# Optimization experiments

Measured on AMD Instinct MI355X. Metric: run time of the kernel, lower is better.

The kernel has to match this reference:

```python
import jax, jax.numpy as jnp
import numpy as np

B, S, HID, NH, DH, L, FF = 1, 4096, 768, 12, 64, 12, 3072
WIN = 256       # one-sided sliding window (attention_window = 512 total)
NG = 16         # number of global-attention tokens
VOCAB = 50265
NEG = -1e9


def layer_norm(x, g, b, eps=1e-5):
    mu = jnp.mean(x, -1, keepdims=True)
    var = jnp.mean((x - mu) ** 2, -1, keepdims=True)
    return (x - mu) * jax.lax.rsqrt(var + eps) * g + b


def forward(input_ids, attention_mask, global_attention_mask, tok_emb, pos_emb,
            emb_ln_w, emb_ln_b, Wqkv, bqkv, Wo, bo, ln1_w, ln1_b,
            W1, b1, W2, b2, ln2_w, ln2_b, cls_W, cls_b):
    c = WIN
    nc = S // c
    amask = attention_mask.astype(jnp.float32)          # [B,S]
    gmask = global_attention_mask.astype(jnp.float32)   # [B,S]

    # --- static-shape helpers for the sparse pattern ---
    # key chunk k covers padded positions [k*c, k*c + 3c)
    idx = (jnp.arange(nc) * c)[:, None] + jnp.arange(3 * c)[None, :]      # [nc,3c]
    diff = jnp.arange(3 * c)[None, :] - c - jnp.arange(c)[:, None]        # [c,3c]
    band = jnp.abs(diff) <= c
    mp = jnp.pad(amask, ((0, 0), (c, c)))[:, idx]                         # [B,nc,3c]
    gp = jnp.pad(gmask, ((0, 0), (c, c)))[:, idx]
    key_ok = (mp > 0) & (gp == 0)           # local keys: valid and not global (globals handled separately)
    loc_valid = band[None, None] & key_ok[:, :, None, :]                  # [B,nc,c,3c]

    # indices of the NG global tokens (earliest first)
    _, gidx = jax.lax.top_k(gmask * (2.0 * S) - jnp.arange(S, dtype=jnp.float32), NG)
    gvalid = jnp.take_along_axis(gmask, gidx, axis=1)                     # [B,NG]

    def attn(x, Wqkv_l, bqkv_l, Wo_l, bo_l):
        qkv = x @ Wqkv_l + bqkv_l
        q, k, v = jnp.split(qkv, 3, axis=-1)
        hd = lambda t: t.reshape(B, S, NH, DH).transpose(0, 2, 1, 3)      # [B,nh,S,dh]
        q = hd(q) * (DH ** -0.5); k = hd(k); v = hd(v)

        # sliding-window (banded) attention via overlapping key chunks
        kp = jnp.pad(k, ((0, 0), (0, 0), (c, c), (0, 0)))
        vp = jnp.pad(v, ((0, 0), (0, 0), (c, c), (0, 0)))
        Kc, Vc = kp[:, :, idx], vp[:, :, idx]                             # [B,nh,nc,3c,dh]
        Qc = q.reshape(B, NH, nc, c, DH)
        s_loc = jnp.einsum('bhkpd,bhkqd->bhkpq', Qc, Kc)                  # [B,nh,nc,c,3c]
        s_loc = jnp.where(loc_valid[:, None], s_loc, NEG)

        # every token also attends to the global tokens
        gi = jnp.broadcast_to(gidx[:, None, :, None], (B, NH, NG, DH))
        Kg = jnp.take_along_axis(k, gi, axis=2)                           # [B,nh,NG,dh]
        Vg = jnp.take_along_axis(v, gi, axis=2)
        Qg = jnp.take_along_axis(q, gi, axis=2)
        s_glb = jnp.einsum('bhkpd,bhgd->bhkpg', Qc, Kg)                   # [B,nh,nc,c,NG]
        s_glb = jnp.where(gvalid[:, None, None, None, :] > 0, s_glb, NEG)

        p = jax.nn.softmax(jnp.concatenate([s_loc, s_glb], -1), axis=-1)
        o = (jnp.einsum('bhkpq,bhkqd->bhkpd', p[..., :3 * c], Vc)
             + jnp.einsum('bhkpg,bhgd->bhkpd', p[..., 3 * c:], Vg))
        o = o.reshape(B, NH, S, DH).transpose(0, 2, 1, 3)                 # [B,S,nh,dh]

        # global tokens attend to the full sequence
        s_full = jnp.einsum('bhgd,bhsd->bhgs', Qg, k)
        s_full = jnp.where(amask[:, None, None, :] > 0, s_full, NEG)
        og = jnp.einsum('bhgs,bhsd->bhgd', jax.nn.softmax(s_full, -1), v)
        og = og.transpose(0, 2, 1, 3)                                     # [B,NG,nh,dh]
        bi = jnp.arange(B)[:, None]
        o = o.at[bi, gidx].set(jnp.where(gvalid[..., None, None] > 0, og, o[bi, gidx]))
        return o.reshape(B, S, HID) @ Wo_l + bo_l

    h = layer_norm(tok_emb[input_ids] + pos_emb[None], emb_ln_w, emb_ln_b)

    def step(h, p):
        Wq, bq, Wo_l, bo_l, g1, bl1, w1, bb1, w2, bb2, g2, bl2 = p
        h = layer_norm(h + attn(h, Wq, bq, Wo_l, bo_l), g1, bl1)          # post-LN, RoBERTa-style
        f = jax.nn.gelu(h @ w1 + bb1, approximate=False) @ w2 + bb2
        h = layer_norm(h + f, g2, bl2)
        return h, None

    h, _ = jax.lax.scan(step, h, (Wqkv, bqkv, Wo, bo, ln1_w, ln1_b,
                                  W1, b1, W2, b2, ln2_w, ln2_b))
    m = amask[..., None]
    pooled = (h * m).sum(1) / m.sum(1)           # masked mean-pool; dropout is eval no-op
    return pooled @ cls_W + cls_b                # [B,2] logits


def setup_inputs():
    key = jax.random.key(0)
    ks = jax.random.split(key, 8)
    nrm = lambda k, shp: jax.random.normal(k, shp, jnp.float32) * 0.02
    return dict(
        input_ids=jax.random.randint(ks[0], (B, S), 0, VOCAB),
        attention_mask=jnp.ones((B, S), jnp.int32),
        global_attention_mask=jnp.concatenate(
            [jnp.ones((B, NG), jnp.int32), jnp.zeros((B, S - NG), jnp.int32)], axis=1),
        tok_emb=nrm(ks[1], (VOCAB, HID)),
        pos_emb=nrm(ks[2], (S, HID)),
        emb_ln_w=jnp.ones((HID,)), emb_ln_b=jnp.zeros((HID,)),
        Wqkv=nrm(ks[3], (L, HID, 3 * HID)), bqkv=jnp.zeros((L, 3 * HID)),
        Wo=nrm(ks[4], (L, HID, HID)), bo=jnp.zeros((L, HID)),
        ln1_w=jnp.ones((L, HID)), ln1_b=jnp.zeros((L, HID)),
        W1=nrm(ks[5], (L, HID, FF)), b1=jnp.zeros((L, FF)),
        W2=nrm(ks[6], (L, FF, HID)), b2=jnp.zeros((L, HID)),
        ln2_w=jnp.ones((L, HID)), ln2_b=jnp.zeros((L, HID)),
        cls_W=nrm(ks[7], (HID, 2)), cls_b=jnp.zeros((2,)),
    )


def reference(input_ids, attention_mask, global_attention_mask, tok_emb, pos_emb,
              emb_ln_w, emb_ln_b, Wqkv, bqkv, Wo, bo, ln1_w, ln1_b,
              W1, b1, W2, b2, ln2_w, ln2_b, cls_W, cls_b):
    return forward(input_ids, attention_mask, global_attention_mask, tok_emb, pos_emb,
                   emb_ln_w, emb_ln_b, Wqkv, bqkv, Wo, bo, ln1_w, ln1_b,
                   W1, b1, W2, b2, ln2_w, ln2_b, cls_W, cls_b)
```

## Files before the change

kernel.cpp:

```cpp
#include <hip/hip_runtime.h>
#include <cmath>

#define S 4096
#define HID 768
#define NH 12
#define DH 64
#define CHUNK 256
#define NC (S / CHUNK)
#define NG 16
#define FF 3072
#define NLAYER 12
#define QKV3 (3 * HID)
#define NEGV -1e9f

typedef _Float16 f16;
typedef __attribute__((ext_vector_type(2))) _Float16 f16x2;
typedef __attribute__((ext_vector_type(4))) _Float16 f16x4;
typedef __attribute__((ext_vector_type(8))) _Float16 f16x8;
typedef __attribute__((ext_vector_type(4))) float f32x4;

__device__ __forceinline__ void async16(f16* lds, const f16* g) {
  __builtin_amdgcn_global_load_lds((const __attribute__((address_space(1))) unsigned int*)g,
                                   (__attribute__((address_space(3))) unsigned int*)lds,
                                   16, 0, 0);
}

__device__ __forceinline__ int xcd_swz(int lin, int nwg) {
  return (lin & 7) * (nwg >> 3) + (lin >> 3);
}

__device__ __forceinline__ float block_reduce_sum(float v, float* red) {
  int t = threadIdx.x;
  red[t] = v; __syncthreads();
  for (int st = 128; st > 0; st >>= 1) {
    if (t < st) red[t] += red[t + st];
    __syncthreads();
  }
  float r = red[0]; __syncthreads();
  return r;
}

__global__ void gidx_kernel(const int* __restrict__ gmask, int* __restrict__ gidx,
                            float* __restrict__ gvalid) {
  if (threadIdx.x != 0 || blockIdx.x != 0) return;
  int cnt = 0;
  for (int s = 0; s < S && cnt < NG; s++)
    if (gmask[s] > 0) { gidx[cnt] = s; gvalid[cnt] = 1.f; cnt++; }
  for (int s = 0; s < S && cnt < NG; s++)
    if (gmask[s] == 0) { gidx[cnt] = s; gvalid[cnt] = 0.f; cnt++; }
}

__global__ __launch_bounds__(256) void embed_ln_kernel(
    const int* __restrict__ ids, const float* __restrict__ tok,
    const float* __restrict__ pos, const float* __restrict__ g,
    const float* __restrict__ b, f16* __restrict__ h16) {
  int s = blockIdx.x, t = threadIdx.x;
  __shared__ float xs[HID];
  __shared__ float red[256];
  const float* tr = tok + (size_t)ids[s] * HID;
  const float* pr = pos + (size_t)s * HID;
  float ls = 0.f;
  for (int i = t; i < HID; i += 256) { float v = tr[i] + pr[i]; xs[i] = v; ls += v; }
  float mu = block_reduce_sum(ls, red) * (1.f / HID);
  float lv = 0.f;
  for (int i = t; i < HID; i += 256) { float d = xs[i] - mu; lv += d * d; }
  float var = block_reduce_sum(lv, red) * (1.f / HID);
  float inv = rsqrtf(var + 1e-5f);
  for (int i = t; i < HID; i += 256)
    h16[(size_t)s * HID + i] = (f16)((xs[i] - mu) * inv * g[i] + b[i]);
}

__global__ __launch_bounds__(256) void ln_kernel(
    const f16* __restrict__ sum16, const float* __restrict__ g,
    const float* __restrict__ b, f16* __restrict__ h16) {
  int s = blockIdx.x, t = threadIdx.x;
  __shared__ float red[256];
  float x0 = (float)sum16[(size_t)s * HID + t];
  float x1 = (float)sum16[(size_t)s * HID + t + 256];
  float x2 = (float)sum16[(size_t)s * HID + t + 512];
  float mu = block_reduce_sum(x0 + x1 + x2, red) * (1.f / HID);
  float d0 = x0 - mu, d1 = x1 - mu, d2 = x2 - mu;
  float var = block_reduce_sum(d0 * d0 + d1 * d1 + d2 * d2, red) * (1.f / HID);
  float inv = rsqrtf(var + 1e-5f);
  h16[(size_t)s * HID + t] = (f16)(d0 * inv * g[t] + b[t]);
  h16[(size_t)s * HID + t + 256] = (f16)(d1 * inv * g[t + 256] + b[t + 256]);
  h16[(size_t)s * HID + t + 512] = (f16)(d2 * inv * g[t + 512] + b[t + 512]);
}

__global__ __launch_bounds__(256) void wt_kernel(const float* __restrict__ W,
                                                 f16* __restrict__ WT, int K, int N) {
  size_t lo = (size_t)blockIdx.z * K * N;
  const float* Wl = W + lo;
  f16* WTl = WT + lo;
  __shared__ float tile[32][33];
  int k0 = blockIdx.y * 32, n0 = blockIdx.x * 32;
  int t = threadIdx.x;
  int r = t >> 3, c = (t & 7) * 4;
  float4 v = *(const float4*)&Wl[(size_t)(k0 + r) * N + n0 + c];
  tile[r][c] = v.x; tile[r][c + 1] = v.y; tile[r][c + 2] = v.z; tile[r][c + 3] = v.w;
  __syncthreads();
  int n = t >> 3, kq = (t & 7) * 4;
  f16x4 o = {(f16)tile[kq][n], (f16)tile[kq + 1][n], (f16)tile[kq + 2][n], (f16)tile[kq + 3][n]};
  *(f16x4*)&WTl[(size_t)(n0 + n) * K + k0 + kq] = o;
}

#define GBK 64

template <bool GELU>
__global__ __launch_bounds__(256) void gemm_f16_kernel(
    const f16* __restrict__ A, const f16* __restrict__ BT,
    const float* __restrict__ bias, f16* __restrict__ Cout, int M, int N, int K) {
  __shared__ f16 As[128 * GBK];
  __shared__ f16 Bs[128 * GBK];
  int t = threadIdx.x, lane = t & 63, wave = t >> 6;
  int wr = wave >> 1, wc = wave & 1;
  int gx = gridDim.x;
  int nl = xcd_swz(blockIdx.y * gx + blockIdx.x, gx * gridDim.y);
  int bx = nl % gx, by = nl / gx;

  f32x4 acc[4][4];
#pragma unroll
  for (int mi = 0; mi < 4; mi++)
#pragma unroll
    for (int ni = 0; ni < 4; ni++) acc[mi][ni] = (f32x4){0.f, 0.f, 0.f, 0.f};

  const f16* Ablk = A + (size_t)(by * 128) * K;
  const f16* Bblk = BT + (size_t)(bx * 128) * K;
  int rl = lane >> 3;
  int lc = (lane & 7) ^ rl;

  for (int k0 = 0; k0 < K; k0 += GBK) {
#pragma unroll
    for (int ii = 0; ii < 4; ii++) {
      int i = wave * 4 + ii;
      int r = i * 8 + rl;
      async16(&As[i * 512], Ablk + (size_t)r * K + k0 + lc * 8);
      async16(&Bs[i * 512], Bblk + (size_t)r * K + k0 + lc * 8);
    }
    __syncthreads();
#pragma unroll
    for (int kc = 0; kc < 2; kc++) {
      f16x8 af[4], bf[4];
#pragma unroll
      for (int mi = 0; mi < 4; mi++) {
        int row = wr * 64 + mi * 16 + (lane & 15);
        int pc = (kc * 4 + (lane >> 4)) ^ (row & 7);
        af[mi] = *(const f16x8*)&As[row * 64 + pc * 8];
      }
#pragma unroll
      for (int ni = 0; ni < 4; ni++) {
        int row = wc * 64 + ni * 16 + (lane & 15);
        int pc = (kc * 4 + (lane >> 4)) ^ (row & 7);
        bf[ni] = *(const f16x8*)&Bs[row * 64 + pc * 8];
      }
#pragma unroll
      for (int mi = 0; mi < 4; mi++)
#pragma unroll
        for (int ni = 0; ni < 4; ni++)
          acc[mi][ni] = __builtin_amdgcn_mfma_f32_16x16x32_f16(af[mi], bf[ni], acc[mi][ni], 0, 0, 0);
    }
    __syncthreads();
  }

  int row_base = by * 128 + wr * 64 + (lane >> 4) * 4;
  int col_base = bx * 128 + wc * 64 + (lane & 15);
#pragma unroll
  for (int mi = 0; mi < 4; mi++) {
#pragma unroll
    for (int ni = 0; ni < 4; ni++) {
      int col = col_base + ni * 16;
      float bs = bias[col];
#pragma unroll
      for (int j = 0; j < 4; j++) {
        int row = row_base + mi * 16 + j;
        float x = acc[mi][ni][j] + bs;
        if (GELU) x = 0.5f * x * (1.f + erff(x * 0.70710678118654752f));
        Cout[(size_t)row * N + col] = (f16)x;
      }
    }
  }
}

template <bool RESID>
__global__ __launch_bounds__(256) void gemm_f16_n64_kernel(
    const f16* __restrict__ A, const f16* __restrict__ BT,
    const float* __restrict__ bias, const f16* __restrict__ resid,
    f16* __restrict__ Cout, int M, int N, int K) {
  __shared__ f16 As[128 * GBK];
  __shared__ f16 Bs[64 * GBK];
  int t = threadIdx.x, lane = t & 63, wave = t >> 6;
  int wr = wave >> 1, wc = wave & 1;
  int gx = gridDim.x;
  int nl = xcd_swz(blockIdx.y * gx + blockIdx.x, gx * gridDim.y);
  int bx = nl % gx, by = nl / gx;

  f32x4 acc[4][2];
#pragma unroll
  for (int mi = 0; mi < 4; mi++)
#pragma unroll
    for (int ni = 0; ni < 2; ni++) acc[mi][ni] = (f32x4){0.f, 0.f, 0.f, 0.f};

  const f16* Ablk = A + (size_t)(by * 128) * K;
  const f16* Bblk = BT + (size_t)(bx * 64) * K;
  int rl = lane >> 3;
  int lc = (lane & 7) ^ rl;

  for (int k0 = 0; k0 < K; k0 += GBK) {
#pragma unroll
    for (int ii = 0; ii < 4; ii++) {
      int i = wave * 4 + ii;
      int r = i * 8 + rl;
      async16(&As[i * 512], Ablk + (size_t)r * K + k0 + lc * 8);
    }
#pragma unroll
    for (int ii = 0; ii < 2; ii++) {
      int i = wave * 2 + ii;
      int r = i * 8 + rl;
      async16(&Bs[i * 512], Bblk + (size_t)r * K + k0 + lc * 8);
    }
    __syncthreads();
#pragma unroll
    for (int kc = 0; kc < 2; kc++) {
      f16x8 af[4], bf[2];
#pragma unroll
      for (int mi = 0; mi < 4; mi++) {
        int row = wr * 64 + mi * 16 + (lane & 15);
        int pc = (kc * 4 + (lane >> 4)) ^ (row & 7);
        af[mi] = *(const f16x8*)&As[row * 64 + pc * 8];
      }
#pragma unroll
      for (int ni = 0; ni < 2; ni++) {
        int row = wc * 32 + ni * 16 + (lane & 15);
        int pc = (kc * 4 + (lane >> 4)) ^ (row & 7);
        bf[ni] = *(const f16x8*)&Bs[row * 64 + pc * 8];
      }
#pragma unroll
      for (int mi = 0; mi < 4; mi++)
#pragma unroll
        for (int ni = 0; ni < 2; ni++)
          acc[mi][ni] = __builtin_amdgcn_mfma_f32_16x16x32_f16(af[mi], bf[ni], acc[mi][ni], 0, 0, 0);
    }
    __syncthreads();
  }

  int row_base = by * 128 + wr * 64 + (lane >> 4) * 4;
  int col_base = bx * 64 + wc * 32 + (lane & 15);
#pragma unroll
  for (int mi = 0; mi < 4; mi++) {
#pragma unroll
    for (int ni = 0; ni < 2; ni++) {
      int col = col_base + ni * 16;
      float bs = bias[col];
#pragma unroll
      for (int j = 0; j < 4; j++) {
        int row = row_base + mi * 16 + j;
        float x = acc[mi][ni][j] + bs;
        if (RESID) x += (float)resid[(size_t)row * N + col];
        Cout[(size_t)row * N + col] = (f16)x;
      }
    }
  }
}

#define ROWP 72

__global__ __launch_bounds__(256) void local_attn_mfma_kernel(
    const f16* __restrict__ qkv, const int* __restrict__ amask,
    const int* __restrict__ gmask, const int* __restrict__ gidx,
    const float* __restrict__ gvalid, f16* __restrict__ outp) {
  int nl = xcd_swz(blockIdx.x, NH * 64);
  int h = nl >> 6;
  int qb = nl & 63;
  int q0 = qb * 64;
  int t = threadIdx.x, lane = t & 63, w = t >> 6;
  int g4 = lane >> 4, l15 = lane & 15;

  __shared__ f16 Qs[64 * ROWP];
  __shared__ f16 Kt[64 * ROWP];
  __shared__ f16 Vt[64 * ROWP];
  __shared__ f16 Pb[4 * 16 * ROWP];
  __shared__ unsigned kokLo, kokHi;
  __shared__ float gvs[NG];

  {
    int r = t >> 2, c2 = (t & 3) * 2;
    const f16* qr = qkv + (size_t)(q0 + r) * QKV3 + h * DH + c2 * 8;
    f16x8 v0 = *(const f16x8*)qr;
    f16x8 v1 = *(const f16x8*)(qr + 8);
#pragma unroll
    for (int e = 0; e < 8; e++) { v0[e] = v0[e] * (f16)0.125f; v1[e] = v1[e] * (f16)0.125f; }
    *(f16x8*)&Qs[r * ROWP + c2 * 8] = v0;
    *(f16x8*)&Qs[r * ROWP + c2 * 8 + 8] = v1;
    if (t < NG) gvs[t] = gvalid[t];
  }
  __syncthreads();

  int qrow = w * 16 + l15;
  f16x8 qf0 = *(const f16x8*)&Qs[qrow * ROWP + g4 * 8];
  f16x8 qf1 = *(const f16x8*)&Qs[qrow * ROWP + 32 + g4 * 8];

  float mb = -50000.f, lp = 0.f;
  f32x4 oacc[4];
#pragma unroll
  for (int sd = 0; sd < 4; sd++) oacc[sd] = (f32x4){0.f, 0.f, 0.f, 0.f};

  f16* Pw = &Pb[w * 16 * ROWP];

  for (int kt = 0; kt <= 9; kt++) {
    int jb = q0 - 256 + kt * 64;
    bool isG = (kt == 9);
    if (!isG && (jb + 64 <= 0 || jb >= S)) continue;
    __syncthreads();
    {
      int k = t >> 2, c2 = (t & 3) * 2;
      int j = isG ? (k < NG ? gidx[k] : -1) : (jb + k);
      bool jv = isG ? (k < NG && gvs[k] > 0.f) : (j >= 0 && j < S);
      f16x8 v0 = {}, v1 = {};
      if (jv) {
        const f16* kr = qkv + (size_t)j * QKV3 + HID + h * DH + c2 * 8;
        v0 = *(const f16x8*)kr; v1 = *(const f16x8*)(kr + 8);
      }
      *(f16x8*)&Kt[k * ROWP + c2 * 8] = v0;
      *(f16x8*)&Kt[k * ROWP + c2 * 8 + 8] = v1;
    }
    if (w == 0) {
      int k = lane;
      bool ok;
      if (isG) ok = (k < NG && gvs[k] > 0.f);
      else {
        int j = jb + k;
        ok = (j >= 0 && j < S) && (amask[j] != 0) && (gmask[j] == 0);
      }
      unsigned long long m = __ballot(ok);
      if (lane == 0) { kokLo = (unsigned)m; kokHi = (unsigned)(m >> 32); }
    }
    {
      int k2 = (t & 31) * 2, dq = (t >> 5) * 8;
      int j0 = isG ? (k2 < NG ? gidx[k2] : -1) : (jb + k2);
      int j1 = isG ? (k2 + 1 < NG ? gidx[k2 + 1] : -1) : (jb + k2 + 1);
      bool ok0 = isG ? (k2 < NG && gvs[k2] > 0.f) : (j0 >= 0 && j0 < S);
      bool ok1 = isG ? (k2 + 1 < NG && gvs[k2 + 1] > 0.f) : (j1 >= 0 && j1 < S);
      f16x8 va = {}, vb = {};
      if (ok0) va = *(const f16x8*)(qkv + (size_t)j0 * QKV3 + 2 * HID + h * DH + dq);
      if (ok1) vb = *(const f16x8*)(qkv + (size_t)j1 * QKV3 + 2 * HID + h * DH + dq);
#pragma unroll
      for (int e = 0; e < 8; e++) {
        f16x2 pr = {va[e], vb[e]};
        *(f16x2*)&Vt[(dq + e) * ROWP + k2] = pr;
      }
    }
    __syncthreads();

    unsigned long long kok = ((unsigned long long)kokHi << 32) | (unsigned long long)kokLo;

    f32x4 sv[4];
    __builtin_amdgcn_s_setprio(1);
#pragma unroll
    for (int s4 = 0; s4 < 4; s4++) {
      int krow = s4 * 16 + l15;
      f16x8 ka0 = *(const f16x8*)&Kt[krow * ROWP + g4 * 8];
      f16x8 ka1 = *(const f16x8*)&Kt[krow * ROWP + 32 + g4 * 8];
      f32x4 a = {0.f, 0.f, 0.f, 0.f};
      a = __builtin_amdgcn_mfma_f32_16x16x32_f16(ka0, qf0, a, 0, 0, 0);
      a = __builtin_amdgcn_mfma_f32_16x16x32_f16(ka1, qf1, a, 0, 0, 0);
      sv[s4] = a;
    }
    __builtin_amdgcn_s_setprio(0);
    int ql = w * 16 + l15;
#pragma unroll
    for (int s4 = 0; s4 < 4; s4++)
#pragma unroll
      for (int r = 0; r < 4; r++) {
        int kl = s4 * 16 + g4 * 4 + r;
        bool ok = (kok >> kl) & 1ull;
        if (kt == 0) ok = ok && (kl >= ql);
        else if (kt == 8) ok = ok && (kl <= ql);
        sv[s4][r] = ok ? sv[s4][r] : -1e30f;
      }
    float mt = -1e30f;
#pragma unroll
    for (int s4 = 0; s4 < 4; s4++)
#pragma unroll
      for (int r = 0; r < 4; r++) mt = fmaxf(mt, sv[s4][r]);
    mt = fmaxf(mt, __shfl_xor(mt, 16));
    mt = fmaxf(mt, __shfl_xor(mt, 32));
    float mn = fmaxf(mb, mt);
    float corr = __expf(mb - mn);
    mb = mn;
    lp *= corr;
#pragma unroll
    for (int sd = 0; sd < 4; sd++)
#pragma unroll
      for (int r = 0; r < 4; r++) oacc[sd][r] *= corr;
#pragma unroll
    for (int s4 = 0; s4 < 4; s4++) {
#pragma unroll
      for (int rp = 0; rp < 2; rp++) {
        float p0 = __expf(sv[s4][rp * 2] - mn);
        float p1 = __expf(sv[s4][rp * 2 + 1] - mn);
        f16 h0 = (f16)p0, h1 = (f16)p1;
        lp += (float)h0 + (float)h1;
        int kl = s4 * 16 + g4 * 4 + rp * 2;
        f16x2 pr = {h0, h1};
        *(f16x2*)&Pw[l15 * ROWP + kl] = pr;
      }
    }
    f16x8 pf0 = *(const f16x8*)&Pw[l15 * ROWP + g4 * 8];
    f16x8 pf1 = *(const f16x8*)&Pw[l15 * ROWP + 32 + g4 * 8];
    __builtin_amdgcn_s_setprio(1);
#pragma unroll
    for (int sd = 0; sd < 4; sd++) {
      int drow = sd * 16 + l15;
      f16x8 va0 = *(const f16x8*)&Vt[drow * ROWP + g4 * 8];
      f16x8 va1 = *(const f16x8*)&Vt[drow * ROWP + 32 + g4 * 8];
      oacc[sd] = __builtin_amdgcn_mfma_f32_16x16x32_f16(va0, pf0, oacc[sd], 0, 0, 0);
      oacc[sd] = __builtin_amdgcn_mfma_f32_16x16x32_f16(va1, pf1, oacc[sd], 0, 0, 0);
    }
    __builtin_amdgcn_s_setprio(0);
  }

  float lt = lp + __shfl_xor(lp, 16);
  lt = lt + __shfl_xor(lt, 32);
  float inv = (lt > 0.f) ? 1.f / lt : 0.f;
  int qg = q0 + w * 16 + l15;
  f16* orow = outp + (size_t)qg * HID + h * DH;
#pragma unroll
  for (int sd = 0; sd < 4; sd++)
#pragma unroll
    for (int r = 0; r < 4; r++)
      orow[sd * 16 + g4 * 4 + r] = (f16)(oacc[sd][r] * inv);
}

__global__ __launch_bounds__(256) void gscore_kernel(
    const f16* __restrict__ qkv, const int* __restrict__ amask,
    const int* __restrict__ gidx, float* __restrict__ Sg, float2* __restrict__ cstat) {
  int h = blockIdx.x >> 4, jc = blockIdx.x & 15;
  int t = threadIdx.x, lane = t & 63, w = t >> 6;
  __shared__ f16 Qs[NG][DH];
  __shared__ float wred[4][NG];
  __shared__ float cmaxs[NG];
  if (t < 128) {
    int g = t >> 3, c = (t & 7) * 8;
    const f16* qr = qkv + (size_t)gidx[g] * QKV3 + h * DH + c;
    *(f16x8*)&Qs[g][c] = *(const f16x8*)qr;
  }
  __syncthreads();
  int j = jc * 256 + t;
  const f16x8* kr = (const f16x8*)(qkv + (size_t)j * QKV3 + HID + h * DH);
  f16x8 kv[8];
#pragma unroll
  for (int c = 0; c < 8; c++) kv[c] = kr[c];
  bool ok = amask[j] != 0;
  float sg[NG];
#pragma unroll 4
  for (int g = 0; g < NG; g++) {
    float s = 0.f;
#pragma unroll
    for (int c = 0; c < 8; c++) {
      f16x8 qv = *(const f16x8*)&Qs[g][c * 8];
#pragma unroll
      for (int e = 0; e < 8; e++) s += (float)qv[e] * (float)kv[c][e];
    }
    sg[g] = ok ? s * 0.125f : NEGV;
    Sg[(size_t)(h * NG + g) * S + j] = sg[g];
  }
#pragma unroll
  for (int g = 0; g < NG; g++) {
    float m = sg[g];
#pragma unroll
    for (int st = 1; st < 64; st <<= 1) m = fmaxf(m, __shfl_xor(m, st));
    if (lane == 0) wred[w][g] = m;
  }
  __syncthreads();
  if (t < NG)
    cmaxs[t] = fmaxf(fmaxf(wred[0][t], wred[1][t]), fmaxf(wred[2][t], wred[3][t]));
  __syncthreads();
#pragma unroll
  for (int g = 0; g < NG; g++) {
    float p = __expf(sg[g] - cmaxs[g]);
#pragma unroll
    for (int st = 1; st < 64; st <<= 1) p += __shfl_xor(p, st);
    if (lane == 0) wred[w][g] = p;
  }
  __syncthreads();
  if (t < NG) {
    float s4 = wred[0][t] + wred[1][t] + wred[2][t] + wred[3][t];
    cstat[((size_t)(h * NG + t)) * 16 + jc] = make_float2(cmaxs[t], s4);
  }
}

__global__ __launch_bounds__(256) void gpv_kernel(
    const f16* __restrict__ qkv, const float* __restrict__ Sg,
    const float2* __restrict__ cstat, float* __restrict__ part) {
  int h = blockIdx.x >> 4, jc = blockIdx.x & 15;
  int jb = jc * 256;
  int t = threadIdx.x;
  __shared__ float Ps[NG][256];
  __shared__ f16 Vs[256][DH];
  __shared__ float ms[NG], dinv[NG];
  if (t < NG) {
    const float2* cs = &cstat[((size_t)(h * NG + t)) * 16];
    float m = -1e30f;
#pragma unroll
    for (int c = 0; c < 16; c++) m = fmaxf(m, cs[c].x);
    float den = 0.f;
#pragma unroll
    for (int c = 0; c < 16; c++) den += cs[c].y * __expf(cs[c].x - m);
    ms[t] = m;
    dinv[t] = den > 0.f ? 1.f / den : 0.f;
  }
  __syncthreads();
#pragma unroll
  for (int g = 0; g < NG; g++)
    Ps[g][t] = __expf(Sg[(size_t)(h * NG + g) * S + jb + t] - ms[g]) * dinv[g];
  {
    int r = t >> 3, c = (t & 7) * 8;
#pragma unroll
    for (int pp = 0; pp < 8; pp++) {
      int row = pp * 32 + r;
      const f16* vr = qkv + (size_t)(jb + row) * QKV3 + 2 * HID + h * DH + c;
      *(f16x8*)&Vs[row][c] = *(const f16x8*)vr;
    }
  }
  __syncthreads();
  int d = t & 63, g4 = t >> 6;
  float o0 = 0.f, o1 = 0.f, o2 = 0.f, o3 = 0.f;
#pragma unroll 8
  for (int j = 0; j < 256; j++) {
    float v = (float)Vs[j][d];
    o0 += Ps[g4][j] * v;
    o1 += Ps[g4 + 4][j] * v;
    o2 += Ps[g4 + 8][j] * v;
    o3 += Ps[g4 + 12][j] * v;
  }
  size_t base = ((size_t)h * NG) * 16 * 64;
  part[base + ((size_t)(g4) * 16 + jc) * 64 + d] = o0;
  part[base + ((size_t)(g4 + 4) * 16 + jc) * 64 + d] = o1;
  part[base + ((size_t)(g4 + 8) * 16 + jc) * 64 + d] = o2;
  part[base + ((size_t)(g4 + 12) * 16 + jc) * 64 + d] = o3;
}

__global__ __launch_bounds__(64) void gout_kernel(
    const float* __restrict__ part, const int* __restrict__ gidx,
    const float* __restrict__ gvalid, f16* __restrict__ attn16) {
  int h = blockIdx.x >> 4, g = blockIdx.x & 15;
  if (gvalid[g] <= 0.f) return;
  int d = threadIdx.x;
  const float* pr = part + (((size_t)(h * NG + g)) * 16) * 64 + d;
  float s = 0.f;
#pragma unroll
  for (int jc = 0; jc < 16; jc++) s += pr[jc * 64];
  attn16[(size_t)gidx[g] * HID + h * DH + d] = (f16)s;
}

__global__ __launch_bounds__(256) void pool_part_kernel(
    const f16* __restrict__ h, const int* __restrict__ amask, float* __restrict__ part) {
  int b = blockIdx.x, t = threadIdx.x;
  float a0 = 0.f, a1 = 0.f, a2 = 0.f;
  for (int r = 0; r < 64; r++) {
    int s = b * 64 + r;
    float w = (float)amask[s];
    const f16* hr = h + (size_t)s * HID;
    a0 += (float)hr[t] * w;
    a1 += (float)hr[t + 256] * w;
    a2 += (float)hr[t + 512] * w;
  }
  part[(size_t)b * HID + t] = a0;
  part[(size_t)b * HID + t + 256] = a1;
  part[(size_t)b * HID + t + 512] = a2;
}

__global__ __launch_bounds__(256) void cls_head_kernel(
    const float* __restrict__ part, const int* __restrict__ amask,
    const float* __restrict__ clsW, const float* __restrict__ clsb,
    float* __restrict__ out) {
  __shared__ float pooled[HID];
  __shared__ float red[256];
  int t = threadIdx.x;
  for (int i = t; i < HID; i += 256) {
    float s = 0.f;
    for (int b2 = 0; b2 < 64; b2++) s += part[(size_t)b2 * HID + i];
    pooled[i] = s;
  }
  float c = 0.f;
  for (int s2 = t; s2 < S; s2 += 256) c += (float)amask[s2];
  float cnt = block_reduce_sum(c, red);
  float p0 = 0.f, p1 = 0.f;
  for (int i = t; i < HID; i += 256) {
    float pv = pooled[i] / cnt;
    p0 += pv * clsW[i * 2];
    p1 += pv * clsW[i * 2 + 1];
  }
  float s0 = block_reduce_sum(p0, red);
  float s1 = block_reduce_sum(p1, red);
  if (t == 0) { out[0] = s0 + clsb[0]; out[1] = s1 + clsb[1]; }
}

extern "C" void kernel_launch(void* const* d_in, const int* in_sizes, int n_in,
                              void* d_out, int out_size, void* d_ws, size_t ws_size,
                              hipStream_t stream) {
  const int* ids = (const int*)d_in[0];
  const int* amask = (const int*)d_in[1];
  const int* gmask = (const int*)d_in[2];
  const float* tok = (const float*)d_in[3];
  const float* pos = (const float*)d_in[4];
  const float* elnw = (const float*)d_in[5];
  const float* elnb = (const float*)d_in[6];
  const float* Wqkv = (const float*)d_in[7];
  const float* bqkv = (const float*)d_in[8];
  const float* Wo = (const float*)d_in[9];
  const float* bo = (const float*)d_in[10];
  const float* ln1w = (const float*)d_in[11];
  const float* ln1b = (const float*)d_in[12];
  const float* W1 = (const float*)d_in[13];
  const float* b1 = (const float*)d_in[14];
  const float* W2 = (const float*)d_in[15];
  const float* b2 = (const float*)d_in[16];
  const float* ln2w = (const float*)d_in[17];
  const float* ln2b = (const float*)d_in[18];
  const float* clsW = (const float*)d_in[19];
  const float* clsb = (const float*)d_in[20];

  char* w8 = (char*)d_ws;
  size_t o = 0;
  f16* h16 = (f16*)(w8 + o); o += (size_t)S * HID * 2;
  f16* qkv16 = (f16*)(w8 + o); o += (size_t)S * QKV3 * 2;
  f16* attn16 = (f16*)(w8 + o); o += (size_t)S * HID * 2;
  f16* ff16 = (f16*)(w8 + o); o += (size_t)S * FF * 2;
  f16* sum16 = (f16*)(w8 + o); o += (size_t)S * HID * 2;
  float* part = (float*)(w8 + o); o += (size_t)64 * HID * 4;
  int* gidx = (int*)(w8 + o); o += 64;
  float* gvalid = (float*)(w8 + o); o += 64;
  f16* WqkvT = (f16*)(w8 + o); o += (size_t)NLAYER * HID * QKV3 * 2;
  f16* WoT = (f16*)(w8 + o); o += (size_t)NLAYER * HID * HID * 2;
  f16* W1T = (f16*)(w8 + o); o += (size_t)NLAYER * HID * FF * 2;
  f16* W2T = (f16*)(w8 + o); o += (size_t)NLAYER * FF * HID * 2;
  float* Sg = (float*)(w8 + o); o += (size_t)NH * NG * S * 4;
  float2* cstat = (float2*)(w8 + o); o += (size_t)NH * NG * 16 * 8;
  float* gpart = (float*)(w8 + o); o += (size_t)NH * NG * 16 * 64 * 4;

  gidx_kernel<<<1, 64, 0, stream>>>(gmask, gidx, gvalid);
  embed_ln_kernel<<<S, 256, 0, stream>>>(ids, tok, pos, elnw, elnb, h16);
  wt_kernel<<<dim3(QKV3 / 32, HID / 32, NLAYER), 256, 0, stream>>>(Wqkv, WqkvT, HID, QKV3);
  wt_kernel<<<dim3(HID / 32, HID / 32, NLAYER), 256, 0, stream>>>(Wo, WoT, HID, HID);
  wt_kernel<<<dim3(FF / 32, HID / 32, NLAYER), 256, 0, stream>>>(W1, W1T, HID, FF);
  wt_kernel<<<dim3(HID / 32, FF / 32, NLAYER), 256, 0, stream>>>(W2, W2T, FF, HID);

  for (int l = 0; l < NLAYER; l++) {
    gemm_f16_kernel<false><<<dim3(QKV3 / 128, S / 128), 256, 0, stream>>>(
        h16, WqkvT + (size_t)l * HID * QKV3, bqkv + (size_t)l * QKV3, qkv16, S, QKV3, HID);
    local_attn_mfma_kernel<<<NH * 64, 256, 0, stream>>>(
        qkv16, amask, gmask, gidx, gvalid, attn16);
    gscore_kernel<<<NH * 16, 256, 0, stream>>>(qkv16, amask, gidx, Sg, cstat);
    gpv_kernel<<<NH * 16, 256, 0, stream>>>(qkv16, Sg, cstat, gpart);
    gout_kernel<<<NH * NG, 64, 0, stream>>>(gpart, gidx, gvalid, attn16);
    gemm_f16_n64_kernel<true><<<dim3(HID / 64, S / 128), 256, 0, stream>>>(
        attn16, WoT + (size_t)l * HID * HID, bo + (size_t)l * HID, h16, sum16, S, HID, HID);
    ln_kernel<<<S, 256, 0, stream>>>(sum16, ln1w + (size_t)l * HID, ln1b + (size_t)l * HID, h16);
    gemm_f16_kernel<true><<<dim3(FF / 128, S / 128), 256, 0, stream>>>(
        h16, W1T + (size_t)l * HID * FF, b1 + (size_t)l * FF, ff16, S, FF, HID);
    gemm_f16_n64_kernel<true><<<dim3(HID / 64, S / 128), 256, 0, stream>>>(
        ff16, W2T + (size_t)l * FF * HID, b2 + (size_t)l * HID, h16, sum16, S, HID, FF);
    ln_kernel<<<S, 256, 0, stream>>>(sum16, ln2w + (size_t)l * HID, ln2b + (size_t)l * HID, h16);
  }
  pool_part_kernel<<<64, 256, 0, stream>>>(h16, amask, part);
  cls_head_kernel<<<1, 256, 0, stream>>>(part, amask, clsW, clsb, (float*)d_out);
}
```

Measured before the change: 2.547 ms.

## Split-K the FFN2 GEMM with fused reduce+LN, and prefetch attention K/V tiles

Result: faster. 2.332 ms (-8.5%).

```diff
diff --git a/kernel.cpp b/kernel.cpp
--- a/kernel.cpp
+++ b/kernel.cpp
@@ -87,6 +87,27 @@
   h16[(size_t)s * HID + t + 512] = (f16)(d2 * inv * g[t + 512] + b[t + 512]);
 }
 
+__global__ __launch_bounds__(256) void ln_ffn2_kernel(
+    const f16* __restrict__ p0, const f16* __restrict__ p1,
+    const float* __restrict__ bias, const float* __restrict__ g,
+    const float* __restrict__ b, f16* __restrict__ h16) {
+  int s = blockIdx.x, t = threadIdx.x;
+  __shared__ float red[256];
+  size_t base = (size_t)s * HID;
+  float x0 = (float)p0[base + t] + (float)p1[base + t] + bias[t] + (float)h16[base + t];
+  float x1 = (float)p0[base + t + 256] + (float)p1[base + t + 256] + bias[t + 256] +
+             (float)h16[base + t + 256];
+  float x2 = (float)p0[base + t + 512] + (float)p1[base + t + 512] + bias[t + 512] +
+             (float)h16[base + t + 512];
+  float mu = block_reduce_sum(x0 + x1 + x2, red) * (1.f / HID);
+  float d0 = x0 - mu, d1 = x1 - mu, d2 = x2 - mu;
+  float var = block_reduce_sum(d0 * d0 + d1 * d1 + d2 * d2, red) * (1.f / HID);
+  float inv = rsqrtf(var + 1e-5f);
+  h16[base + t] = (f16)(d0 * inv * g[t] + b[t]);
+  h16[base + t + 256] = (f16)(d1 * inv * g[t + 256] + b[t + 256]);
+  h16[base + t + 512] = (f16)(d2 * inv * g[t + 512] + b[t + 512]);
+}
+
 __global__ __launch_bounds__(256) void wt_kernel(const float* __restrict__ W,
                                                  f16* __restrict__ WT, int K, int N) {
   size_t lo = (size_t)blockIdx.z * K * N;
@@ -262,7 +283,114 @@
   }
 }
 
+__global__ __launch_bounds__(256) void gemm_f16_n64_splitk_kernel(
+    const f16* __restrict__ A, const f16* __restrict__ BT,
+    f16* __restrict__ p0, f16* __restrict__ p1, int M, int N, int K) {
+  __shared__ f16 As[128 * GBK];
+  __shared__ f16 Bs[64 * GBK];
+  int t = threadIdx.x, lane = t & 63, wave = t >> 6;
+  int wr = wave >> 1, wc = wave & 1;
+  int gx = gridDim.x;
+  int nl = xcd_swz(blockIdx.y * gx + blockIdx.x, gx * gridDim.y);
+  int bx = nl % gx, by = nl / gx;
+  int kz = blockIdx.z;
+  int KH = K >> 1;
+  f16* pout = kz ? p1 : p0;
+
+  f32x4 acc[4][2];
+#pragma unroll
+  for (int mi = 0; mi < 4; mi++)
+#pragma unroll
+    for (int ni = 0; ni < 2; ni++) acc[mi][ni] = (f32x4){0.f, 0.f, 0.f, 0.f};
+
+  const f16* Ablk = A + (size_t)(by * 128) * K + (size_t)kz * KH;
+  const f16* Bblk = BT + (size_t)(bx * 64) * K + (size_t)kz * KH;
+  int rl = lane >> 3;
+  int lc = (lane & 7) ^ rl;
+
+  for (int k0 = 0; k0 < KH; k0 += GBK) {
+#pragma unroll
+    for (int ii = 0; ii < 4; ii++) {
+      int i = wave * 4 + ii;
+      int r = i * 8 + rl;
+      async16(&As[i * 512], Ablk + (size_t)r * K + k0 + lc * 8);
+    }
+#pragma unroll
+    for (int ii = 0; ii < 2; ii++) {
+      int i = wave * 2 + ii;
+      int r = i * 8 + rl;
+      async16(&Bs[i * 512], Bblk + (size_t)r * K + k0 + lc * 8);
+    }
+    __syncthreads();
+#pragma unroll
+    for (int kc = 0; kc < 2; kc++) {
+      f16x8 af[4], bf[2];
+#pragma unroll
+      for (int mi = 0; mi < 4; mi++) {
+        int row = wr * 64 + mi * 16 + (lane & 15);
+        int pc = (kc * 4 + (lane >> 4)) ^ (row & 7);
+        af[mi] = *(const f16x8*)&As[row * 64 + pc * 8];
+      }
+#pragma unroll
+      for (int ni = 0; ni < 2; ni++) {
+        int row = wc * 32 + ni * 16 + (lane & 15);
+        int pc = (kc * 4 + (lane >> 4)) ^ (row & 7);
+        bf[ni] = *(const f16x8*)&Bs[row * 64 + pc * 8];
+      }
+#pragma unroll
+      for (int mi = 0; mi < 4; mi++)
+#pragma unroll
+        for (int ni = 0; ni < 2; ni++)
+          acc[mi][ni] = __builtin_amdgcn_mfma_f32_16x16x32_f16(af[mi], bf[ni], acc[mi][ni], 0, 0, 0);
+    }
+    __syncthreads();
+  }
+
+  int row_base = by * 128 + wr * 64 + (lane >> 4) * 4;
+  int col_base = bx * 64 + wc * 32 + (lane & 15);
+#pragma unroll
+  for (int mi = 0; mi < 4; mi++) {
+#pragma unroll
+    for (int ni = 0; ni < 2; ni++) {
+      int col = col_base + ni * 16;
+#pragma unroll
+      for (int j = 0; j < 4; j++) {
+        int row = row_base + mi * 16 + j;
+        pout[(size_t)row * N + col] = (f16)acc[mi][ni][j];
+      }
+    }
+  }
+}
+
 #define ROWP 72
+
+__device__ __forceinline__ void pf_load(
+    const f16* __restrict__ qkv, const int* __restrict__ gidx, const float* gvs,
+    int h, int q0, int kt, int t,
+    f16x8& pk0, f16x8& pk1, f16x8& pva, f16x8& pvb) {
+  int jb = q0 - 256 + kt * 64;
+  bool isG = (kt == 9);
+  pk0 = (f16x8){}; pk1 = (f16x8){}; pva = (f16x8){}; pvb = (f16x8){};
+  int kr = t >> 2, c2 = (t & 3) * 2;
+  bool kok_;
+  int jk;
+  if (isG) { kok_ = (kr < NG) && (gvs[kr] > 0.f); jk = kok_ ? gidx[kr] : 0; }
+  else { kok_ = true; jk = jb + kr; }
+  if (kok_) {
+    const f16* kp = qkv + (size_t)jk * QKV3 + HID + h * DH + c2 * 8;
+    pk0 = *(const f16x8*)kp;
+    pk1 = *(const f16x8*)(kp + 8);
+  }
+  int k2 = (t & 31) * 2, dq = (t >> 5) * 8;
+  bool o0, o1;
+  int j0, j1;
+  if (isG) {
+    o0 = (k2 < NG) && (gvs[k2] > 0.f); j0 = o0 ? gidx[k2] : 0;
+    o1 = (k2 + 1 < NG) && (gvs[k2 + 1] > 0.f); j1 = o1 ? gidx[k2 + 1] : 0;
+  } else { o0 = o1 = true; j0 = jb + k2; j1 = jb + k2 + 1; }
+  if (o0) pva = *(const f16x8*)(qkv + (size_t)j0 * QKV3 + 2 * HID + h * DH + dq);
+  if (o1) pvb = *(const f16x8*)(qkv + (size_t)j1 * QKV3 + 2 * HID + h * DH + dq);
+}
 
 __global__ __launch_bounds__(256) void local_attn_mfma_kernel(
     const f16* __restrict__ qkv, const int* __restrict__ amask,
@@ -306,22 +434,31 @@
 
   f16* Pw = &Pb[w * 16 * ROWP];
 
-  for (int kt = 0; kt <= 9; kt++) {
+  int kt_lo = q0 >= 256 ? 0 : (256 - q0) >> 6;
+  int kt_hi = (4288 - q0) >> 6;
+  if (kt_hi > 8) kt_hi = 8;
+  int ntile = kt_hi - kt_lo + 2;
+
+  f16x8 pk0, pk1, pva, pvb;
+  pf_load(qkv, gidx, gvs, h, q0, kt_lo, t, pk0, pk1, pva, pvb);
+
+  for (int it = 0; it < ntile; it++) {
+    int kt = (it < ntile - 1) ? kt_lo + it : 9;
     int jb = q0 - 256 + kt * 64;
     bool isG = (kt == 9);
-    if (!isG && (jb + 64 <= 0 || jb >= S)) continue;
     __syncthreads();
     {
-      int k = t >> 2, c2 = (t & 3) * 2;
-      int j = isG ? (k < NG ? gidx[k] : -1) : (jb + k);
-      bool jv = isG ? (k < NG && gvs[k] > 0.f) : (j >= 0 && j < S);
-      f16x8 v0 = {}, v1 = {};
-      if (jv) {
-        const f16* kr = qkv + (size_t)j * QKV3 + HID + h * DH + c2 * 8;
-        v0 = *(const f16x8*)kr; v1 = *(const f16x8*)(kr + 8);
-      }
-      *(f16x8*)&Kt[k * ROWP + c2 * 8] = v0;
-      *(f16x8*)&Kt[k * ROWP + c2 * 8 + 8] = v1;
+      int kr = t >> 2, c2 = (t & 3) * 2;
+      *(f16x8*)&Kt[kr * ROWP + c2 * 8] = pk0;
+      *(f16x8*)&Kt[kr * ROWP + c2 * 8 + 8] = pk1;
+    }
+    {
+      int k2 = (t & 31) * 2, dq = (t >> 5) * 8;
+#pragma unroll
+      for (int e = 0; e < 8; e++) {
+        f16x2 pr = {pva[e], pvb[e]};
+        *(f16x2*)&Vt[(dq + e) * ROWP + k2] = pr;
+      }
     }
     if (w == 0) {
       int k = lane;
@@ -329,25 +466,14 @@
       if (isG) ok = (k < NG && gvs[k] > 0.f);
       else {
         int j = jb + k;
-        ok = (j >= 0 && j < S) && (amask[j] != 0) && (gmask[j] == 0);
+        ok = (amask[j] != 0) && (gmask[j] == 0);
       }
       unsigned long long m = __ballot(ok);
       if (lane == 0) { kokLo = (unsigned)m; kokHi = (unsigned)(m >> 32); }
     }
-    {
-      int k2 = (t & 31) * 2, dq = (t >> 5) * 8;
-      int j0 = isG ? (k2 < NG ? gidx[k2] : -1) : (jb + k2);
-      int j1 = isG ? (k2 + 1 < NG ? gidx[k2 + 1] : -1) : (jb + k2 + 1);
-      bool ok0 = isG ? (k2 < NG && gvs[k2] > 0.f) : (j0 >= 0 && j0 < S);
-      bool ok1 = isG ? (k2 + 1 < NG && gvs[k2 + 1] > 0.f) : (j1 >= 0 && j1 < S);
-      f16x8 va = {}, vb = {};
-      if (ok0) va = *(const f16x8*)(qkv + (size_t)j0 * QKV3 + 2 * HID + h * DH + dq);
-      if (ok1) vb = *(const f16x8*)(qkv + (size_t)j1 * QKV3 + 2 * HID + h * DH + dq);
-#pragma unroll
-      for (int e = 0; e < 8; e++) {
-        f16x2 pr = {va[e], vb[e]};
-        *(f16x2*)&Vt[(dq + e) * ROWP + k2] = pr;
-      }
+    if (it + 1 < ntile) {
+      int ktn = (it + 1 < ntile - 1) ? kt_lo + it + 1 : 9;
+      pf_load(qkv, gidx, gvs, h, q0, ktn, t, pk0, pk1, pva, pvb);
     }
     __syncthreads();
 
@@ -628,6 +754,7 @@
   f16* attn16 = (f16*)(w8 + o); o += (size_t)S * HID * 2;
   f16* ff16 = (f16*)(w8 + o); o += (size_t)S * FF * 2;
   f16* sum16 = (f16*)(w8 + o); o += (size_t)S * HID * 2;
+  f16* p1 = (f16*)(w8 + o); o += (size_t)S * HID * 2;
   float* part = (float*)(w8 + o); o += (size_t)64 * HID * 4;
   int* gidx = (int*)(w8 + o); o += 64;
   float* gvalid = (float*)(w8 + o); o += 64;
@@ -659,9 +786,10 @@
     ln_kernel<<<S, 256, 0, stream>>>(sum16, ln1w + (size_t)l * HID, ln1b + (size_t)l * HID, h16);
     gemm_f16_kernel<true><<<dim3(FF / 128, S / 128), 256, 0, stream>>>(
         h16, W1T + (size_t)l * HID * FF, b1 + (size_t)l * FF, ff16, S, FF, HID);
-    gemm_f16_n64_kernel<true><<<dim3(HID / 64, S / 128), 256, 0, stream>>>(
-        ff16, W2T + (size_t)l * FF * HID, b2 + (size_t)l * HID, h16, sum16, S, HID, FF);
-    ln_kernel<<<S, 256, 0, stream>>>(sum16, ln2w + (size_t)l * HID, ln2b + (size_t)l * HID, h16);
+    gemm_f16_n64_splitk_kernel<<<dim3(HID / 64, S / 128, 2), 256, 0, stream>>>(
+        ff16, W2T + (size_t)l * FF * HID, sum16, p1, S, HID, FF);
+    ln_ffn2_kernel<<<S, 256, 0, stream>>>(sum16, p1, b2 + (size_t)l * HID,
+                                          ln2w + (size_t)l * HID, ln2b + (size_t)l * HID, h16);
   }
   pool_part_kernel<<<64, 256, 0, stream>>>(h16, amask, part);
   cls_head_kernel<<<1, 256, 0, stream>>>(part, amask, clsW, clsb, (float*)d_out);
```
